# Kernel optimization log

Hardware: AMD Instinct MI355X
Metric: run time of the kernel (lower is better)

## Reference

```python
import jax, jax.numpy as jnp
import numpy as np

B, S, H, V, A = 64, 512, 1024, 32000, 16
MAX_LEN = 2 * 512 + 2  # 2*TEST_SEQ_LENGTH + 2


def setup_inputs() -> dict:
    key = jax.random.key(0)
    ks = jax.random.split(key, 8)
    sc_h = 1.0 / np.sqrt(H)
    return {
        "x": jax.random.randint(ks[0], (B, S), 0, V),
        "true_actions": jax.random.randint(ks[1], (B, S), 0, A),
        "true_states": jax.random.randint(ks[2], (B, S), 0, A),
        "use_forcing": 0,
        "embed_tok": jax.random.normal(ks[3], (V, H), jnp.float32) * 0.02,
        "embed_pos": jax.random.normal(ks[4], (MAX_LEN, H), jnp.float32) * 0.02,
        "Wi": jax.random.normal(ks[5], (H, 4 * H), jnp.float32) * sc_h,
        "Wh": jax.random.normal(ks[6], (H, 4 * H), jnp.float32) * sc_h,
        "bh": jnp.zeros((4 * H,), jnp.float32),
        "Wd": jax.random.normal(ks[7], (H, A), jnp.float32) * sc_h,
        "bd": jnp.zeros((A,), jnp.float32),
    }


def reference(x, true_actions, true_states, use_forcing,
              embed_tok, embed_pos, Wi, Wh, bh, Wd, bd):
    batch, seq = x.shape
    # token + positional embedding
    xe = embed_tok[x] + embed_pos[jnp.arange(seq)][None, :, :]  # [B,S,H]
    # precompute input contribution to all gates (hoisted out of the scan)
    xi = jnp.einsum('bsh,hg->bsg', xe, Wi)  # [B,S,4H]

    def step(carry, xt):
        c, h = carry
        z = xt + h @ Wh + bh                      # [B,4H]
        i, f, g, o = jnp.split(z, 4, axis=-1)     # flax gate order i,f,g,o
        c = jax.nn.sigmoid(f) * c + jax.nn.sigmoid(i) * jnp.tanh(g)
        h = jax.nn.sigmoid(o) * jnp.tanh(c)
        return (c, h), h

    c0 = jnp.zeros((batch, H), xi.dtype)
    h0 = jnp.zeros((batch, H), xi.dtype)
    _, hs = jax.lax.scan(step, (c0, h0), jnp.swapaxes(xi, 0, 1))  # [S,B,H]
    hs = jnp.swapaxes(hs, 0, 1)  # [B,S,H]

    logits_buf = hs @ Wd + bd  # [B,S,A]
    dummy = jnp.zeros((batch, seq, 1), logits_buf.dtype)
    return (dummy, logits_buf, dummy)
```

## Files before the change

### kernel.cpp

```cpp
#include <hip/hip_runtime.h>
#include <hip/hip_bf16.h>

#define BB 64
#define SS 512
#define HH 1024
#define G4 4096

using bf8_t = __attribute__((ext_vector_type(8))) short;
using f32x4 = __attribute__((ext_vector_type(4))) float;

__device__ inline ushort f2bf(float f) {
  __hip_bfloat16 h = __float2bfloat16(f);
  return *reinterpret_cast<ushort*>(&h);
}
__device__ inline float bf2f(ushort u) {
  unsigned v = ((unsigned)u) << 16;
  return __uint_as_float(v);
}

__global__ __launch_bounds__(256) void k_transpose_cast(
    const float* __restrict__ in, ushort* __restrict__ out, int R, int C) {
  __shared__ float tile[32][33];
  int c0 = blockIdx.x * 32, r0 = blockIdx.y * 32;
  int tx = threadIdx.x & 31, ty = threadIdx.x >> 5;
  for (int i = ty; i < 32; i += 8) {
    int r = r0 + i, c = c0 + tx;
    tile[i][tx] = (r < R && c < C) ? in[(size_t)r * C + c] : 0.f;
  }
  __syncthreads();
  for (int i = ty; i < 32; i += 8) {
    int c = c0 + i, r = r0 + tx;
    if (c < C && r < R) out[(size_t)c * R + r] = f2bf(tile[tx][i]);
  }
}

__global__ __launch_bounds__(256) void k_embed(
    const int* __restrict__ x, const float* __restrict__ etok,
    const float* __restrict__ epos, ushort* __restrict__ Ae) {
  int row = blockIdx.x;
  int t = row >> 6, b = row & 63;
  int tok = x[b * SS + t];
  const float4* tp = (const float4*)(etok + (size_t)tok * HH);
  const float4* pp = (const float4*)(epos + (size_t)t * HH);
  int i = threadIdx.x;
  float4 a = tp[i], p = pp[i];
  ushort4 r = make_ushort4(f2bf(a.x + p.x), f2bf(a.y + p.y),
                           f2bf(a.z + p.z), f2bf(a.w + p.w));
  ((ushort4*)(Ae + (size_t)row * HH))[i] = r;
}

__global__ __launch_bounds__(256) void k_gemm_xi(
    const ushort* __restrict__ Ag, const ushort* __restrict__ Bt,
    const float* __restrict__ bias, ushort* __restrict__ Cout, int N) {
  __shared__ alignas(16) ushort As[128 * 40];
  __shared__ alignas(16) ushort Bs[128 * 40];
  const int m0 = blockIdx.y * 128, n0 = blockIdx.x * 128;
  const int tid = threadIdx.x;
  const int srow = tid >> 1, shalf = tid & 1;
  const int w = tid >> 6, lane = tid & 63;
  const int wm = w >> 1, wn = w & 1;
  const int lr = lane & 15, kq = lane >> 4;
  f32x4 acc[4][4] = {};
  for (int k0 = 0; k0 < HH; k0 += 32) {
    const uint4* ga = (const uint4*)(Ag + (size_t)(m0 + srow) * HH + k0 + shalf * 16);
    const uint4* gb = (const uint4*)(Bt + (size_t)(n0 + srow) * HH + k0 + shalf * 16);
    uint4 va0 = ga[0], va1 = ga[1];
    uint4 vb0 = gb[0], vb1 = gb[1];
    __syncthreads();
    *(uint4*)&As[srow * 40 + shalf * 16]     = va0;
    *(uint4*)&As[srow * 40 + shalf * 16 + 8] = va1;
    *(uint4*)&Bs[srow * 40 + shalf * 16]     = vb0;
    *(uint4*)&Bs[srow * 40 + shalf * 16 + 8] = vb1;
    __syncthreads();
    bf8_t fa[4], fb[4];
#pragma unroll
    for (int i = 0; i < 4; ++i) {
      fa[i] = *(const bf8_t*)&As[(wm * 64 + i * 16 + lr) * 40 + kq * 8];
      fb[i] = *(const bf8_t*)&Bs[(wn * 64 + i * 16 + lr) * 40 + kq * 8];
    }
#pragma unroll
    for (int mi = 0; mi < 4; ++mi)
#pragma unroll
      for (int ni = 0; ni < 4; ++ni)
        acc[mi][ni] = __builtin_amdgcn_mfma_f32_16x16x32_bf16(fa[mi], fb[ni], acc[mi][ni], 0, 0, 0);
  }
#pragma unroll
  for (int mi = 0; mi < 4; ++mi) {
    int grow = m0 + wm * 64 + mi * 16 + kq * 4;
#pragma unroll
    for (int ni = 0; ni < 4; ++ni) {
      int gcol = n0 + wn * 64 + ni * 16 + lr;
      float bv = bias[gcol];
#pragma unroll
      for (int r = 0; r < 4; ++r)
        Cout[(size_t)(grow + r) * N + gcol] = f2bf(acc[mi][ni][r] + bv);
    }
  }
}

__global__ __launch_bounds__(256, 1) void k_recur(
    const ushort* __restrict__ Wh_t,
    const ushort* __restrict__ xi,
    ushort* __restrict__ hs,
    uint4* __restrict__ fragA,
    const uint4* __restrict__ zfrag,
    unsigned* __restrict__ arrive) {
  __shared__ alignas(16) ushort htile[2048 * 8];
  __shared__ alignas(16) float zbuf[4][16][17];
  const int grp = blockIdx.x >> 6;
  const int mem = blockIdx.x & 63;
  const int n0 = mem * 16;
  const int brow0 = grp * 16;
  const int tid = threadIdx.x;
  unsigned* flags = arrive + grp * 64;
  const int w = tid >> 6, lane = tid & 63;
  const int lr = lane & 15, kq = lane >> 4;

  bf8_t fbr[32];
  {
    const ushort* wrow = Wh_t + (size_t)(w * 1024 + n0 + lr) * HH + kq * 8;
#pragma unroll
    for (int k = 0; k < 32; ++k) fbr[k] = *(const bf8_t*)(wrow + k * 32);
#pragma unroll
    for (int k = 0; k < 32; ++k) asm volatile("" : "+v"(fbr[k]));
  }

  const int eb = lane >> 2, en4 = (lane & 3) * 4;
  const int pc = n0 + en4;
  const int pk = pc >> 5, pkq = (pc >> 3) & 3;
  const int pubu = pk * 64 + pkq * 16 + eb;
  const int pubb = (pc & 7) * 2;
  float cr[4] = {0.f, 0.f, 0.f, 0.f};

  ushort4 xv[4] = {};
  if (w == 0) {
    const ushort* xb = xi + ((size_t)brow0 + eb) * G4 + pc;
#pragma unroll
    for (int g = 0; g < 4; ++g) xv[g] = *(const ushort4*)(xb + (size_t)g * 1024);
  }

  for (int t = 0; t < SS; ++t) {
    if (t > 0) {
      if (w == 0) {
        while (__hip_atomic_load(flags + lane, __ATOMIC_RELAXED,
                                 __HIP_MEMORY_SCOPE_AGENT) < (unsigned)t)
          __builtin_amdgcn_s_sleep(1);
      }
      __syncthreads();
      __builtin_amdgcn_fence(__ATOMIC_ACQUIRE, "workgroup");
    }

    const uint4* fsrc = (t == 0) ? (zfrag + grp * 2048)
                                 : (fragA + ((size_t)(t - 1) * 4 + grp) * 2048);
    uint4 hv[8];
#pragma unroll
    for (int i = 0; i < 8; ++i) hv[i] = fsrc[tid + 256 * i];

#pragma unroll
    for (int i = 0; i < 8; ++i) *(uint4*)&htile[(tid + 256 * i) * 8] = hv[i];
    __syncthreads();

    ushort4 xn[4] = {};
    if (w == 0) {
      int tn = (t + 1 < SS) ? t + 1 : t;
      const ushort* xb = xi + ((size_t)tn * 64 + brow0 + eb) * G4 + pc;
#pragma unroll
      for (int g = 0; g < 4; ++g) xn[g] = *(const ushort4*)(xb + (size_t)g * 1024);
    }

    f32x4 acc0 = {}, acc1 = {};
#pragma unroll
    for (int k = 0; k < 32; k += 2) {
      bf8_t fa0 = *(const bf8_t*)&htile[(k * 64 + lane) * 8];
      bf8_t fa1 = *(const bf8_t*)&htile[((k + 1) * 64 + lane) * 8];
      acc0 = __builtin_amdgcn_mfma_f32_16x16x32_bf16(fa0, fbr[k], acc0, 0, 0, 0);
      acc1 = __builtin_amdgcn_mfma_f32_16x16x32_bf16(fa1, fbr[k + 1], acc1, 0, 0, 0);
    }
#pragma unroll
    for (int r = 0; r < 4; ++r)
      zbuf[w][kq * 4 + r][lr] = acc0[r] + acc1[r];
    __syncthreads();

    if (w == 0) {
      f32x4 zi4 = *(const f32x4*)&zbuf[0][eb][en4];
      f32x4 zf4 = *(const f32x4*)&zbuf[1][eb][en4];
      f32x4 zg4 = *(const f32x4*)&zbuf[2][eb][en4];
      f32x4 zo4 = *(const f32x4*)&zbuf[3][eb][en4];
      union { unsigned long long u64; ushort u16[4]; uint2 u32x2; } ho;
#pragma unroll
      for (int j = 0; j < 4; ++j) {
        float zi = zi4[j] + bf2f(((const ushort*)&xv[0])[j]);
        float zf = zf4[j] + bf2f(((const ushort*)&xv[1])[j]);
        float zg = zg4[j] + bf2f(((const ushort*)&xv[2])[j]);
        float zo = zo4[j] + bf2f(((const ushort*)&xv[3])[j]);
        float si = 1.f / (1.f + __expf(-zi));
        float sf = 1.f / (1.f + __expf(-zf));
        float tg = tanhf(zg);
        float so = 1.f / (1.f + __expf(-zo));
        float c = sf * cr[j] + si * tg;
        cr[j] = c;
        ho.u16[j] = f2bf(so * tanhf(c));
      }
      unsigned long long* fdst =
          (unsigned long long*)((char*)(fragA + ((size_t)t * 4 + grp) * 2048) +
                                pubu * 16 + pubb);
      unsigned long long old = __hip_atomic_exchange(
          fdst, ho.u64, __ATOMIC_RELAXED, __HIP_MEMORY_SCOPE_AGENT);
      asm volatile("" :: "v"(old));
      asm volatile("s_waitcnt vmcnt(0)" ::: "memory");
      if (t + 1 < SS && lane == 0)
        __hip_atomic_store(flags + mem, (unsigned)(t + 1),
                           __ATOMIC_RELAXED, __HIP_MEMORY_SCOPE_AGENT);
      *(uint2*)(hs + (size_t)(t + 1) * BB * HH +
                (size_t)(brow0 + eb) * HH + pc) = ho.u32x2;
      xv[0] = xn[0]; xv[1] = xn[1]; xv[2] = xn[2]; xv[3] = xn[3];
    }
  }
}

__global__ __launch_bounds__(256) void k_logits(
    const ushort* __restrict__ hs1, const ushort* __restrict__ Wdt,
    const float* __restrict__ bd, float* __restrict__ out) {
  int gid = blockIdx.x * 256 + threadIdx.x;
  int a = gid & 15, row = gid >> 4;
  int t = row >> 6, b = row & 63;
  const uint4* hp = (const uint4*)(hs1 + (size_t)row * HH);
  const uint4* wp = (const uint4*)(Wdt + (size_t)a * HH);
  float sum = 0.f;
#pragma unroll 4
  for (int i = 0; i < HH / 8; ++i) {
    uint4 hv = hp[i], wv = wp[i];
    const uint* hu = (const uint*)&hv;
    const uint* wu = (const uint*)&wv;
#pragma unroll
    for (int j = 0; j < 4; ++j) {
      sum += bf2f((ushort)(hu[j] & 0xffff)) * bf2f((ushort)(wu[j] & 0xffff));
      sum += bf2f((ushort)(hu[j] >> 16)) * bf2f((ushort)(wu[j] >> 16));
    }
  }
  out[32768 + ((size_t)b * SS + t) * 16 + a] = sum + bd[a];
}

extern "C" void kernel_launch(void* const* d_in, const int* in_sizes, int n_in,
                              void* d_out, int out_size, void* d_ws, size_t ws_size,
                              hipStream_t stream) {
  const int*   x    = (const int*)d_in[0];
  const float* etok = (const float*)d_in[4];
  const float* epos = (const float*)d_in[5];
  const float* Wi   = (const float*)d_in[6];
  const float* Wh   = (const float*)d_in[7];
  const float* bh   = (const float*)d_in[8];
  const float* Wd   = (const float*)d_in[9];
  const float* bd   = (const float*)d_in[10];

  char* ws = (char*)d_ws;
  size_t off = 0;
  ushort* Wi_t = (ushort*)(ws + off); off += (size_t)G4 * HH * 2;
  ushort* Wh_t = (ushort*)(ws + off); off += (size_t)G4 * HH * 2;
  ushort* Wd_t = (ushort*)(ws + off); off += 65536;
  char* AeFrag = ws + off;            off += (size_t)512 * 4 * 2048 * 16;
  ushort* Ae   = (ushort*)AeFrag;
  uint4*  fragA = (uint4*)AeFrag;
  ushort* xi   = (ushort*)(ws + off); off += (size_t)BB * SS * G4 * 2;
  ushort* hs   = (ushort*)(ws + off); off += (size_t)(SS + 1) * BB * HH * 2;
  uint4*  zfrag = (uint4*)(ws + off); off += (size_t)4 * 2048 * 16;
  unsigned* arrive = (unsigned*)(ws + off); off += 4 * 64 * 4;

  hipMemsetAsync(d_out, 0, (size_t)out_size * 4, stream);
  hipMemsetAsync(zfrag, 0, (size_t)4 * 2048 * 16, stream);
  hipMemsetAsync(arrive, 0, 4 * 64 * 4, stream);

  dim3 b256(256);
  k_transpose_cast<<<dim3(G4 / 32, HH / 32), b256, 0, stream>>>(Wi, Wi_t, HH, G4);
  k_transpose_cast<<<dim3(G4 / 32, HH / 32), b256, 0, stream>>>(Wh, Wh_t, HH, G4);
  k_transpose_cast<<<dim3(1, HH / 32), b256, 0, stream>>>(Wd, Wd_t, HH, 16);
  k_embed<<<BB * SS, b256, 0, stream>>>(x, etok, epos, Ae);
  k_gemm_xi<<<dim3(G4 / 128, BB * SS / 128), b256, 0, stream>>>(Ae, Wi_t, bh, xi, G4);
  k_recur<<<256, b256, 0, stream>>>(Wh_t, xi, hs, fragA, zfrag, arrive);
  k_logits<<<BB * SS * 16 / 256, b256, 0, stream>>>(hs + (size_t)BB * HH, Wd_t, bd,
                                                    (float*)d_out);
}
```

Baseline: 3.002 ms.

## Replace per-step arrival flags with sentinel-polled data in recurrent kernel

The recurrent kernel no longer waits on per-block arrival counters. It prefills the h-fragment exchange buffer with a sentinel pattern and has each thread poll its own 8-byte chunks until every chunk differs from the sentinel. This removes the vmcnt wait, the flag store and the flag spin from each step's critical path. In exchange it adds a 64 MB memset per call, and it relies on a real bf16 payload never equalling the sentinel and on 64-bit atomic exchanges being visible as whole words.

```diff
diff --git a/kernel.cpp b/kernel.cpp
--- a/kernel.cpp
+++ b/kernel.cpp
@@ -103,16 +103,15 @@
     const ushort* __restrict__ xi,
     ushort* __restrict__ hs,
     uint4* __restrict__ fragA,
-    const uint4* __restrict__ zfrag,
-    unsigned* __restrict__ arrive) {
+    const uint4* __restrict__ zfrag) {
   __shared__ alignas(16) ushort htile[2048 * 8];
   __shared__ alignas(16) float zbuf[4][16][17];
+  const unsigned long long SENT = 0x7F7F7F7F7F7F7F7FULL;
   const int grp = blockIdx.x >> 6;
   const int mem = blockIdx.x & 63;
   const int n0 = mem * 16;
   const int brow0 = grp * 16;
   const int tid = threadIdx.x;
-  unsigned* flags = arrive + grp * 64;
   const int w = tid >> 6, lane = tid & 63;
   const int lr = lane & 15, kq = lane >> 4;
 
@@ -140,24 +139,39 @@
   }
 
   for (int t = 0; t < SS; ++t) {
-    if (t > 0) {
-      if (w == 0) {
-        while (__hip_atomic_load(flags + lane, __ATOMIC_RELAXED,
-                                 __HIP_MEMORY_SCOPE_AGENT) < (unsigned)t)
-          __builtin_amdgcn_s_sleep(1);
+    unsigned long long uvv[16];
+    if (t == 0) {
+      const uint4* fsrc = zfrag + grp * 2048;
+#pragma unroll
+      for (int i = 0; i < 8; ++i) {
+        uint4 v = fsrc[tid + 256 * i];
+        uvv[2 * i]     = ((unsigned long long)v.y << 32) | v.x;
+        uvv[2 * i + 1] = ((unsigned long long)v.w << 32) | v.z;
       }
-      __syncthreads();
-      __builtin_amdgcn_fence(__ATOMIC_ACQUIRE, "workgroup");
-    }
-
-    const uint4* fsrc = (t == 0) ? (zfrag + grp * 2048)
-                                 : (fragA + ((size_t)(t - 1) * 4 + grp) * 2048);
-    uint4 hv[8];
-#pragma unroll
-    for (int i = 0; i < 8; ++i) hv[i] = fsrc[tid + 256 * i];
-
-#pragma unroll
-    for (int i = 0; i < 8; ++i) *(uint4*)&htile[(tid + 256 * i) * 8] = hv[i];
+    } else {
+      const unsigned long long* q =
+          (const unsigned long long*)(fragA + ((size_t)(t - 1) * 4 + grp) * 2048);
+      unsigned pend = 0xFFFFu;
+      do {
+#pragma unroll
+        for (int j = 0; j < 16; ++j) {
+          if (pend & (1u << j)) {
+            unsigned long long v = __hip_atomic_load(
+                q + ((size_t)(tid + 256 * (j >> 1)) * 2 + (j & 1)),
+                __ATOMIC_RELAXED, __HIP_MEMORY_SCOPE_AGENT);
+            if (v != SENT) { uvv[j] = v; pend &= ~(1u << j); }
+          }
+        }
+      } while (pend);
+    }
+
+#pragma unroll
+    for (int i = 0; i < 8; ++i) {
+      uint4 sw;
+      sw.x = (unsigned)uvv[2 * i];     sw.y = (unsigned)(uvv[2 * i] >> 32);
+      sw.z = (unsigned)uvv[2 * i + 1]; sw.w = (unsigned)(uvv[2 * i + 1] >> 32);
+      *(uint4*)&htile[(size_t)(tid + 256 * i) * 8] = sw;
+    }
     __syncthreads();
 
     ushort4 xn[4] = {};
@@ -207,10 +221,6 @@
       unsigned long long old = __hip_atomic_exchange(
           fdst, ho.u64, __ATOMIC_RELAXED, __HIP_MEMORY_SCOPE_AGENT);
       asm volatile("" :: "v"(old));
-      asm volatile("s_waitcnt vmcnt(0)" ::: "memory");
-      if (t + 1 < SS && lane == 0)
-        __hip_atomic_store(flags + mem, (unsigned)(t + 1),
-                           __ATOMIC_RELAXED, __HIP_MEMORY_SCOPE_AGENT);
       *(uint2*)(hs + (size_t)(t + 1) * BB * HH +
                 (size_t)(brow0 + eb) * HH + pc) = ho.u32x2;
       xv[0] = xn[0]; xv[1] = xn[1]; xv[2] = xn[2]; xv[3] = xn[3];
@@ -264,11 +274,9 @@
   ushort* xi   = (ushort*)(ws + off); off += (size_t)BB * SS * G4 * 2;
   ushort* hs   = (ushort*)(ws + off); off += (size_t)(SS + 1) * BB * HH * 2;
   uint4*  zfrag = (uint4*)(ws + off); off += (size_t)4 * 2048 * 16;
-  unsigned* arrive = (unsigned*)(ws + off); off += 4 * 64 * 4;
 
   hipMemsetAsync(d_out, 0, (size_t)out_size * 4, stream);
   hipMemsetAsync(zfrag, 0, (size_t)4 * 2048 * 16, stream);
-  hipMemsetAsync(arrive, 0, 4 * 64 * 4, stream);
 
   dim3 b256(256);
   k_transpose_cast<<<dim3(G4 / 32, HH / 32), b256, 0, stream>>>(Wi, Wi_t, HH, G4);
@@ -276,7 +284,8 @@
   k_transpose_cast<<<dim3(1, HH / 32), b256, 0, stream>>>(Wd, Wd_t, HH, 16);
   k_embed<<<BB * SS, b256, 0, stream>>>(x, etok, epos, Ae);
   k_gemm_xi<<<dim3(G4 / 128, BB * SS / 128), b256, 0, stream>>>(Ae, Wi_t, bh, xi, G4);
-  k_recur<<<256, b256, 0, stream>>>(Wh_t, xi, hs, fragA, zfrag, arrive);
+  hipMemsetAsync(fragA, 0x7F, (size_t)512 * 4 * 2048 * 16, stream);
+  k_recur<<<256, b256, 0, stream>>>(Wh_t, xi, hs, fragA, zfrag);
   k_logits<<<BB * SS * 16 / 256, b256, 0, stream>>>(hs + (size_t)BB * HH, Wd_t, bd,
                                                     (float*)d_out);
 }
```

After: 3.514 ms. 1.17x slower.
